# Optimization experiments

Hardware: AMD Instinct MI355X
Metric: run time of the kernel (lower is better)

The kernel has to match this reference:

```python
import jax, jax.numpy as jnp
import numpy as np

N, C, H, W = 4, 128, 64, 64


def setup_inputs() -> dict:
    key = jax.random.key(0)
    ks = jax.random.split(key, 4)
    s = 1.0 / np.sqrt(C).astype(np.float32)  # conv2d default-init scale
    return {
        "x": jax.random.normal(ks[0], (N, C, H, W), dtype=jnp.float32),
        "Wq": jax.random.normal(ks[1], (C, C), dtype=jnp.float32) * s,
        "bq": jnp.zeros((C,), dtype=jnp.float32),
        "Wk": jax.random.normal(ks[2], (C, C), dtype=jnp.float32) * s,
        "bk": jnp.zeros((C,), dtype=jnp.float32),
        "Wv": jax.random.normal(ks[3], (C, C), dtype=jnp.float32) * s,
        "bv": jnp.zeros((C,), dtype=jnp.float32),
    }


def reference(x, Wq, bq, Wk, bk, Wv, bv):
    n, c, h, w = x.shape
    xf = x.reshape(n, c, h * w)  # [N, C, L], L = H*W
    # 1x1 convs == per-pixel channel mixing
    q = jnp.einsum('oc,ncl->nol', Wq, xf) + bq[:, None]
    k = jnp.einsum('oc,ncl->nol', Wk, xf) + bk[:, None]
    v = jnp.einsum('oc,ncl->nol', Wv, xf) + bv[:, None]
    # scores[l, m] = sum_c k[c,l] * q[c,m]  (matmul(k^T, q))
    scale = jnp.asarray(1.0 / np.sqrt(c), x.dtype)
    scores = jnp.einsum('ncl,ncm->nlm', k, q) * scale  # [N, L, L]
    temp = jax.nn.softmax(scores, axis=-1)
    attn = jnp.einsum('ncl,nlm->ncm', v, temp)  # [N, C, L]
    return x + attn.reshape(n, c, h, w)
```

## Files before the change

### kernel.cpp

```cpp
#include <hip/hip_runtime.h>
#include <hip/hip_bf16.h>
#include <stdint.h>

#define NB 4
#define CH 128
#define LL 4096

typedef __attribute__((ext_vector_type(8))) short short8;
typedef __attribute__((ext_vector_type(4))) short short4b;
typedef __attribute__((ext_vector_type(4))) float floatx4;
typedef __attribute__((ext_vector_type(16))) float floatx16;


static __device__ __forceinline__ short f2bf(float f) {
    uint32_t u = __float_as_uint(f);
    u += 0x7fffu + ((u >> 16) & 1u);
    return (short)(u >> 16);
}
static __device__ __forceinline__ float bf2f(short s) {
    return __uint_as_float(((uint32_t)(uint16_t)s) << 16);
}

__global__ __launch_bounds__(256) void wprep_kernel(
    const float* __restrict__ Wq, const float* __restrict__ Wk,
    const float* __restrict__ Wv, short* __restrict__ Wf)
{
    const int g = blockIdx.x * 256 + threadIdx.x;
    const int mat = g >> 14;
    const int rem = g & 16383;
    const int o   = rem >> 7;
    const int c   = rem & 127;
    const float* W = (mat == 0) ? Wq : (mat == 1) ? Wk : Wv;
    float v = W[o * CH + c];
    if (mat == 1) v *= 0.08838834764831845f;
    Wf[(size_t)mat * 16384 + (o >> 4) * 2048 + (c >> 5) * 512
       + ((c >> 3) & 3) * 128 + (o & 15) * 8 + (c & 7)] = f2bf(v);
}

__global__ __launch_bounds__(256) void proj_kernel(
    const float* __restrict__ x, const short* __restrict__ Wf,
    const float* __restrict__ bq, const float* __restrict__ bk,
    const float* __restrict__ bv,
    short* __restrict__ Qf, short* __restrict__ Kf, short* __restrict__ Vp)
{
    const int i    = blockIdx.x;
    const int n    = (i >> 1) & 3;
    const int lt   = ((i >> 3) << 1) | (i & 1);
    const int l0   = lt << 5;
    const int tid  = threadIdx.x;
    const int wave = tid >> 6;
    const int lane = tid & 63;
    const int quad = lane >> 4;
    const int mc   = lane & 15;

    __shared__ short Xb[32][136];

    {
        const int sl = tid & 31;
        const int cg = tid >> 5;
        const float* xp = x + ((size_t)n * CH + cg * 16) * LL + l0 + sl;
        short8 buf;
        #pragma unroll
        for (int i2 = 0; i2 < 16; ++i2) {
            buf[i2 & 7] = f2bf(xp[(size_t)i2 * LL]);
            if ((i2 & 7) == 7)
                *(short8*)(void*)&Xb[sl][cg * 16 + (i2 & 8)] = buf;
        }
    }
    __syncthreads();

    const int lt2 = wave >> 1;
    const int oh  = wave & 1;
    const int gt  = lt * 2 + lt2;

    short8 xf[4];
    #pragma unroll
    for (int s = 0; s < 4; ++s)
        xf[s] = *(const short8*)(const void*)&Xb[lt2 * 16 + mc][32 * s + quad * 8];

    const size_t obase = ((size_t)n * 256 + gt) * 2048;
    const float scale = 0.08838834764831845f;

    #pragma unroll
    for (int mat = 0; mat < 3; ++mat) {
        const short* Wm = Wf + (size_t)mat * 16384;
        const float* bb = (mat == 0) ? bq : (mat == 1) ? bk : bv;
        const float bscale = (mat == 1) ? scale : 1.0f;
        #pragma unroll
        for (int ot = oh * 4; ot < oh * 4 + 4; ++ot) {
            floatx4 acc = {0.f, 0.f, 0.f, 0.f};
            #pragma unroll
            for (int s = 0; s < 4; ++s)
                acc = __builtin_amdgcn_mfma_f32_16x16x32_bf16(
                    *(const short8*)(const void*)(Wm + ot * 2048 + s * 512 + lane * 8),
                    xf[s], acc, 0, 0, 0);
            const int c0 = ot * 16 + 4 * quad;
            if (mat < 2) {
                short4b pv;
                #pragma unroll
                for (int r = 0; r < 4; ++r)
                    pv[r] = f2bf(acc[r] + bb[c0 + r] * bscale);
                short* dst = ((mat == 0) ? Qf : Kf) + obase
                           + (c0 >> 5) * 512 + ((c0 >> 3) & 3) * 128
                           + mc * 8 + (c0 & 7);
                *(short4b*)(void*)dst = pv;
            } else {
                #pragma unroll
                for (int r = 0; r < 4; ++r)
                    Vp[obase + (c0 + r) * 16 + mc] = f2bf(acc[r] + bb[c0 + r]);
            }
        }
    }
}

__global__ __launch_bounds__(1024) void rowsum_kernel(
    const short* __restrict__ Qf, const short* __restrict__ Kf,
    float* __restrict__ Dv)
{
    const int i    = blockIdx.x;
    const int n    = (i >> 1) & 3;
    const int tq   = ((i >> 3) << 1) | (i & 1);
    const int tid  = threadIdx.x;
    const int wave = tid >> 6;
    const int lane = tid & 63;
    const int quad = lane >> 4;
    const int mc   = lane & 15;
    const int mw   = wave & 7;
    const int th   = wave >> 3;

    __shared__ float Db[16][32];

    const short* Kb = Kf + ((size_t)n * 256 + tq * 4 + th * 2) * 2048 + lane * 8;
    short8 kf[2][4];
    #pragma unroll
    for (int t = 0; t < 2; ++t)
        #pragma unroll
        for (int s = 0; s < 4; ++s)
            kf[t][s] = *(const short8*)(const void*)(Kb + t * 2048 + s * 512);

    const short* Qn = Qf + (size_t)n * 524288 + (size_t)mw * 32 * 2048 + lane * 8;
    float rs[2][4] = {{0.f, 0.f, 0.f, 0.f}, {0.f, 0.f, 0.f, 0.f}};

    short8 qA[4], qB[4];
    #pragma unroll
    for (int s = 0; s < 4; ++s)
        qA[s] = *(const short8*)(const void*)(Qn + s * 512);

    auto qstep = [&](const short8 (&q)[4]) {
        floatx4 a0 = {0.f, 0.f, 0.f, 0.f};
        floatx4 a1 = {0.f, 0.f, 0.f, 0.f};
        #pragma unroll
        for (int s = 0; s < 4; ++s) {
            a0 = __builtin_amdgcn_mfma_f32_16x16x32_bf16(kf[0][s], q[s], a0, 0, 0, 0);
            a1 = __builtin_amdgcn_mfma_f32_16x16x32_bf16(kf[1][s], q[s], a1, 0, 0, 0);
        }
        #pragma unroll
        for (int r = 0; r < 4; ++r) {
            rs[0][r] += __expf(a0[r]);
            rs[1][r] += __expf(a1[r]);
        }
    };

    for (int it = 0; it < 32; it += 2) {
        #pragma unroll
        for (int s = 0; s < 4; ++s)
            qB[s] = *(const short8*)(const void*)(
                Qn + (size_t)((it + 1) & 31) * 2048 + s * 512);
        qstep(qA);
        #pragma unroll
        for (int s = 0; s < 4; ++s)
            qA[s] = *(const short8*)(const void*)(
                Qn + (size_t)((it + 2) & 31) * 2048 + s * 512);
        qstep(qB);
    }

    #pragma unroll
    for (int t = 0; t < 2; ++t)
        #pragma unroll
        for (int r = 0; r < 4; ++r) {
            float v = rs[t][r];
            v += __shfl_xor(v, 1);
            v += __shfl_xor(v, 2);
            v += __shfl_xor(v, 4);
            v += __shfl_xor(v, 8);
            if (mc == 0) Db[wave][t * 16 + quad * 4 + r] = v;
        }
    __syncthreads();
    if (tid < 64) {
        const int lh = tid >> 5, lr = tid & 31;
        float s = 0.f;
        #pragma unroll
        for (int m = 0; m < 8; ++m) s += Db[lh * 8 + m][lr];
        Dv[(size_t)n * 4096 + tq * 64 + tid] = 1.0f / s;
    }
}

__global__ __launch_bounds__(1024) void attn_out_kernel(
    const short* __restrict__ Qf, const short* __restrict__ Kf,
    const short* __restrict__ Vp, const float* __restrict__ Dv,
    const float* __restrict__ x, float* __restrict__ out)
{
    const int i    = blockIdx.x;
    const int n    = (i >> 1) & 3;
    const int mb   = ((i >> 3) << 1) | (i & 1);
    const int m0   = mb << 6;
    const int tid  = threadIdx.x;
    const int wave = tid >> 6;
    const int lane = tid & 63;
    const int quad = lane >> 4;
    const int mc   = lane & 15;
    const int l32  = lane & 31;
    const int h    = lane >> 5;
    const int ct   = wave & 3;
    const int mh   = (wave >> 2) & 1;
    const int kh   = wave >> 3;

    __shared__ short P[2][64][264];
    __shared__ float Rbuf[4][2][64][16];

    const short* Qn  = Qf + (size_t)n * 524288;
    const short* Kn  = Kf + (size_t)n * 524288;
    const short* Vpn = Vp + (size_t)n * 524288;
    const float* Dn  = Dv + (size_t)n * 4096;

    short8 qf[4][4];
    #pragma unroll
    for (int mst = 0; mst < 4; ++mst)
        #pragma unroll
        for (int s = 0; s < 4; ++s)
            qf[mst][s] = *(const short8*)(const void*)(
                Qn + (size_t)((m0 >> 4) + mst) * 2048 + s * 512 + lane * 8);

    floatx16 acc;
    #pragma unroll
    for (int r = 0; r < 16; ++r) acc[r] = 0.f;

    for (int step = 0; step < 16; ++step) {
        const int lb = step << 8;
        const int p  = step & 1;

        short8 kfr[4];
        #pragma unroll
        for (int s = 0; s < 4; ++s)
            kfr[s] = *(const short8*)(const void*)(
                Kn + (size_t)(step * 16 + wave) * 2048 + s * 512 + lane * 8);
        const floatx4 dr = *(const floatx4*)(const void*)(
            Dn + lb + wave * 16 + quad * 4);

        #pragma unroll
        for (int mst = 0; mst < 4; ++mst) {
            floatx4 sa = {0.f, 0.f, 0.f, 0.f};
            #pragma unroll
            for (int s = 0; s < 4; ++s)
                sa = __builtin_amdgcn_mfma_f32_16x16x32_bf16(kfr[s], qf[mst][s], sa, 0, 0, 0);
            short4b pv;
            #pragma unroll
            for (int r = 0; r < 4; ++r) pv[r] = f2bf(__expf(sa[r]) * dr[r]);
            *(short4b*)(void*)&P[p][16 * mst + mc][16 * wave + quad * 4] = pv;
        }
        __syncthreads();

        #pragma unroll
        for (int i2 = 0; i2 < 8; ++i2) {
            const int kc = kh * 8 + i2;
            const short8 vf = *(const short8*)(const void*)(
                Vpn + (size_t)((lb >> 4) + kc) * 2048 + (32 * ct + l32) * 16 + 8 * h);
            const short8 pf = *(const short8*)(const void*)&P[p][32 * mh + l32][16 * kc + 8 * h];
            acc = __builtin_amdgcn_mfma_f32_32x32x16_bf16(vf, pf, acc, 0, 0, 0);
        }
    }

    __syncthreads();
    if (kh == 1)
        *(floatx16*)(void*)&Rbuf[ct][mh][lane][0] = acc;
    __syncthreads();
    if (kh == 0) {
        const floatx16 o = *(const floatx16*)(const void*)&Rbuf[ct][mh][lane][0];
        #pragma unroll
        for (int r = 0; r < 16; ++r) {
            const int c = 32 * ct + (r & 3) + 8 * (r >> 2) + 4 * h;
            const int m = m0 + 32 * mh + l32;
            const size_t idx = ((size_t)n * CH + c) * LL + m;
            out[idx] = x[idx] + acc[r] + o[r];
        }
    }
}

extern "C" void kernel_launch(void* const* d_in, const int* in_sizes, int n_in,
                              void* d_out, int out_size, void* d_ws, size_t ws_size,
                              hipStream_t stream) {
    (void)in_sizes; (void)n_in; (void)out_size; (void)ws_size;
    const float* x  = (const float*)d_in[0];
    const float* Wq = (const float*)d_in[1];
    const float* bq = (const float*)d_in[2];
    const float* Wk = (const float*)d_in[3];
    const float* bk = (const float*)d_in[4];
    const float* Wv = (const float*)d_in[5];
    const float* bv = (const float*)d_in[6];
    float* out = (float*)d_out;

    char* ws = (char*)d_ws;
    short* Qf = (short*)(ws);
    short* Kf = (short*)(ws + 4194304);
    short* Vp = (short*)(ws + 8388608);
    float* Dv = (float*)(ws + 12582912);
    short* Wf = (short*)(ws + 16777216);

    wprep_kernel<<<192, 256, 0, stream>>>(Wq, Wk, Wv, Wf);
    proj_kernel<<<512, 256, 0, stream>>>(x, Wf, bq, bk, bv, Qf, Kf, Vp);
    rowsum_kernel<<<256, 1024, 0, stream>>>(Qf, Kf, Dv);
    attn_out_kernel<<<256, 1024, 0, stream>>>(Qf, Kf, Vp, Dv, x, out);
}
```

Measured before the change: 169.2 us.

## Halve attn_out tile to 32 queries, 512 threads, prefetch next K/D and V

The attention-output kernel now processes 32 query columns per block with 8 waves (512 threads) instead of 64 columns with 16 waves, doubling the grid to 512 blocks. Each step covers 128 keys, and the K fragments and row-sum reciprocals for the next step are loaded during the current step's compute. V fragments are loaded into registers before the score MFMAs, so their latency overlaps with the exp/P work. The reduction buffer now reuses the P shared array. The intent is more blocks per CU and better hiding of global-load latency, at the cost of more register pressure and more total K/V reads, since each block now covers fewer queries.

```diff
diff --git a/kernel.cpp b/kernel.cpp
--- a/kernel.cpp
+++ b/kernel.cpp
@@ -195,7 +195,7 @@
     }
 }
 
-__global__ __launch_bounds__(1024) void attn_out_kernel(
+__global__ __launch_bounds__(512, 4) void attn_out_kernel(
     const short* __restrict__ Qf, const short* __restrict__ Kf,
     const short* __restrict__ Vp, const float* __restrict__ Dv,
     const float* __restrict__ x, float* __restrict__ out)
@@ -203,7 +203,7 @@
     const int i    = blockIdx.x;
     const int n    = (i >> 1) & 3;
     const int mb   = ((i >> 3) << 1) | (i & 1);
-    const int m0   = mb << 6;
+    const int m0   = mb << 5;
     const int tid  = threadIdx.x;
     const int wave = tid >> 6;
     const int lane = tid & 63;
@@ -212,20 +212,19 @@
     const int l32  = lane & 31;
     const int h    = lane >> 5;
     const int ct   = wave & 3;
-    const int mh   = (wave >> 2) & 1;
-    const int kh   = wave >> 3;
-
-    __shared__ short P[2][64][264];
-    __shared__ float Rbuf[4][2][64][16];
+    const int kh   = wave >> 2;
+
+    __shared__ short P[2][32][138];
+    float* Rb = (float*)&P[0][0][0];
 
     const short* Qn  = Qf + (size_t)n * 524288;
     const short* Kn  = Kf + (size_t)n * 524288;
     const short* Vpn = Vp + (size_t)n * 524288;
     const float* Dn  = Dv + (size_t)n * 4096;
 
-    short8 qf[4][4];
-    #pragma unroll
-    for (int mst = 0; mst < 4; ++mst)
+    short8 qf[2][4];
+    #pragma unroll
+    for (int mst = 0; mst < 2; ++mst)
         #pragma unroll
         for (int s = 0; s < 4; ++s)
             qf[mst][s] = *(const short8*)(const void*)(
@@ -235,20 +234,35 @@
     #pragma unroll
     for (int r = 0; r < 16; ++r) acc[r] = 0.f;
 
-    for (int step = 0; step < 16; ++step) {
-        const int lb = step << 8;
+    short8 kfr[4];
+    #pragma unroll
+    for (int s = 0; s < 4; ++s)
+        kfr[s] = *(const short8*)(const void*)(
+            Kn + (size_t)wave * 2048 + s * 512 + lane * 8);
+    floatx4 dr = *(const floatx4*)(const void*)(Dn + wave * 16 + quad * 4);
+
+    for (int step = 0; step < 32; ++step) {
+        const int lb = step << 7;
         const int p  = step & 1;
 
-        short8 kfr[4];
-        #pragma unroll
-        for (int s = 0; s < 4; ++s)
-            kfr[s] = *(const short8*)(const void*)(
-                Kn + (size_t)(step * 16 + wave) * 2048 + s * 512 + lane * 8);
-        const floatx4 dr = *(const floatx4*)(const void*)(
-            Dn + lb + wave * 16 + quad * 4);
-
-        #pragma unroll
-        for (int mst = 0; mst < 4; ++mst) {
+        short8 vf[4];
+        #pragma unroll
+        for (int s = 0; s < 4; ++s)
+            vf[s] = *(const short8*)(const void*)(
+                Vpn + (size_t)((lb >> 4) + kh * 4 + s) * 2048
+                    + (32 * ct + l32) * 16 + 8 * h);
+
+        const int sn = (step + 1) & 31;
+        short8 kfn[4];
+        #pragma unroll
+        for (int s = 0; s < 4; ++s)
+            kfn[s] = *(const short8*)(const void*)(
+                Kn + (size_t)(sn * 8 + wave) * 2048 + s * 512 + lane * 8);
+        const floatx4 dn2 = *(const floatx4*)(const void*)(
+            Dn + (sn << 7) + wave * 16 + quad * 4);
+
+        #pragma unroll
+        for (int mst = 0; mst < 2; ++mst) {
             floatx4 sa = {0.f, 0.f, 0.f, 0.f};
             #pragma unroll
             for (int s = 0; s < 4; ++s)
@@ -261,25 +275,27 @@
         __syncthreads();
 
         #pragma unroll
-        for (int i2 = 0; i2 < 8; ++i2) {
-            const int kc = kh * 8 + i2;
-            const short8 vf = *(const short8*)(const void*)(
-                Vpn + (size_t)((lb >> 4) + kc) * 2048 + (32 * ct + l32) * 16 + 8 * h);
-            const short8 pf = *(const short8*)(const void*)&P[p][32 * mh + l32][16 * kc + 8 * h];
-            acc = __builtin_amdgcn_mfma_f32_32x32x16_bf16(vf, pf, acc, 0, 0, 0);
-        }
+        for (int i2 = 0; i2 < 4; ++i2) {
+            const int kc = kh * 4 + i2;
+            const short8 pf = *(const short8*)(const void*)&P[p][l32][16 * kc + 8 * h];
+            acc = __builtin_amdgcn_mfma_f32_32x32x16_bf16(vf[i2], pf, acc, 0, 0, 0);
+        }
+
+        #pragma unroll
+        for (int s = 0; s < 4; ++s) kfr[s] = kfn[s];
+        dr = dn2;
     }
 
     __syncthreads();
     if (kh == 1)
-        *(floatx16*)(void*)&Rbuf[ct][mh][lane][0] = acc;
+        *(floatx16*)(void*)&Rb[(ct * 64 + lane) * 16] = acc;
     __syncthreads();
     if (kh == 0) {
-        const floatx16 o = *(const floatx16*)(const void*)&Rbuf[ct][mh][lane][0];
+        const floatx16 o = *(const floatx16*)(const void*)&Rb[(ct * 64 + lane) * 16];
         #pragma unroll
         for (int r = 0; r < 16; ++r) {
             const int c = 32 * ct + (r & 3) + 8 * (r >> 2) + 4 * h;
-            const int m = m0 + 32 * mh + l32;
+            const int m = m0 + l32;
             const size_t idx = ((size_t)n * CH + c) * LL + m;
             out[idx] = x[idx] + acc[r] + o[r];
         }
@@ -309,5 +325,5 @@
     wprep_kernel<<<192, 256, 0, stream>>>(Wq, Wk, Wv, Wf);
     proj_kernel<<<512, 256, 0, stream>>>(x, Wf, bq, bk, bv, Qf, Kf, Vp);
     rowsum_kernel<<<256, 1024, 0, stream>>>(Qf, Kf, Dv);
-    attn_out_kernel<<<256, 1024, 0, stream>>>(Qf, Kf, Vp, Dv, x, out);
-}
+    attn_out_kernel<<<512, 512, 0, stream>>>(Qf, Kf, Vp, Dv, x, out);
+}
```

Result: slower. 191.6 us (+13.2%).

## Software-pipeline attention loop: compute next P tile while consuming current

Applied to the files above, without the earlier changes.

Restructures the main loop so that the score/exp tile for step t+1 is computed into the alternate P buffer while the PV MFMAs for step t run, with a prologue that computes the first tile. K and D loads are prefetched two steps ahead and V fragments are loaded into registers ahead of use, and the loop now needs one barrier per iteration instead of sitting on one between the two phases. This aims to hide global-load latency and overlap the two MFMA phases, at the cost of higher register pressure from the extra prefetched fragments, which could reduce occupancy.

```diff
diff --git a/kernel.cpp b/kernel.cpp
--- a/kernel.cpp
+++ b/kernel.cpp
@@ -235,42 +235,93 @@
     #pragma unroll
     for (int r = 0; r < 16; ++r) acc[r] = 0.f;
 
-    for (int step = 0; step < 16; ++step) {
-        const int lb = step << 8;
-        const int p  = step & 1;
-
-        short8 kfr[4];
-        #pragma unroll
-        for (int s = 0; s < 4; ++s)
-            kfr[s] = *(const short8*)(const void*)(
-                Kn + (size_t)(step * 16 + wave) * 2048 + s * 512 + lane * 8);
-        const floatx4 dr = *(const floatx4*)(const void*)(
-            Dn + lb + wave * 16 + quad * 4);
-
-        #pragma unroll
-        for (int mst = 0; mst < 4; ++mst) {
-            floatx4 sa = {0.f, 0.f, 0.f, 0.f};
+    short8 knxt[4];
+    #pragma unroll
+    for (int s = 0; s < 4; ++s)
+        knxt[s] = *(const short8*)(const void*)(
+            Kn + (size_t)wave * 2048 + s * 512 + lane * 8);
+    floatx4 dnxt = *(const floatx4*)(const void*)(Dn + wave * 16 + quad * 4);
+
+    #pragma unroll
+    for (int mst = 0; mst < 4; ++mst) {
+        floatx4 sa = {0.f, 0.f, 0.f, 0.f};
+        #pragma unroll
+        for (int s = 0; s < 4; ++s)
+            sa = __builtin_amdgcn_mfma_f32_16x16x32_bf16(knxt[s], qf[mst][s], sa, 0, 0, 0);
+        short4b pv;
+        #pragma unroll
+        for (int r = 0; r < 4; ++r) pv[r] = f2bf(__expf(sa[r]) * dnxt[r]);
+        *(short4b*)(void*)&P[0][16 * mst + mc][16 * wave + quad * 4] = pv;
+    }
+    #pragma unroll
+    for (int s = 0; s < 4; ++s)
+        knxt[s] = *(const short8*)(const void*)(
+            Kn + (size_t)(16 + wave) * 2048 + s * 512 + lane * 8);
+    dnxt = *(const floatx4*)(const void*)(Dn + 256 + wave * 16 + quad * 4);
+    __syncthreads();
+
+    #pragma unroll 2
+    for (int t = 0; t < 16; ++t) {
+        const int lb = t << 8;
+        const int p  = t & 1;
+
+        short8 vf0[4];
+        #pragma unroll
+        for (int s = 0; s < 4; ++s)
+            vf0[s] = *(const short8*)(const void*)(
+                Vpn + (size_t)((lb >> 4) + kh * 8 + s) * 2048
+                    + (32 * ct + l32) * 16 + 8 * h);
+
+        const int tf = (t + 2 < 16) ? t + 2 : 15;
+        short8 kfut[4];
+        #pragma unroll
+        for (int s = 0; s < 4; ++s)
+            kfut[s] = *(const short8*)(const void*)(
+                Kn + (size_t)(tf * 16 + wave) * 2048 + s * 512 + lane * 8);
+        const floatx4 dfut = *(const floatx4*)(const void*)(
+            Dn + (tf << 8) + wave * 16 + quad * 4);
+
+        if (t < 15) {
             #pragma unroll
-            for (int s = 0; s < 4; ++s)
-                sa = __builtin_amdgcn_mfma_f32_16x16x32_bf16(kfr[s], qf[mst][s], sa, 0, 0, 0);
-            short4b pv;
-            #pragma unroll
-            for (int r = 0; r < 4; ++r) pv[r] = f2bf(__expf(sa[r]) * dr[r]);
-            *(short4b*)(void*)&P[p][16 * mst + mc][16 * wave + quad * 4] = pv;
-        }
+            for (int mst = 0; mst < 4; ++mst) {
+                floatx4 sa = {0.f, 0.f, 0.f, 0.f};
+                #pragma unroll
+                for (int s = 0; s < 4; ++s)
+                    sa = __builtin_amdgcn_mfma_f32_16x16x32_bf16(knxt[s], qf[mst][s], sa, 0, 0, 0);
+                short4b pv;
+                #pragma unroll
+                for (int r = 0; r < 4; ++r) pv[r] = f2bf(__expf(sa[r]) * dnxt[r]);
+                *(short4b*)(void*)&P[p ^ 1][16 * mst + mc][16 * wave + quad * 4] = pv;
+            }
+        }
+
+        short8 vf1[4];
+        #pragma unroll
+        for (int s = 0; s < 4; ++s)
+            vf1[s] = *(const short8*)(const void*)(
+                Vpn + (size_t)((lb >> 4) + kh * 8 + 4 + s) * 2048
+                    + (32 * ct + l32) * 16 + 8 * h);
+
+        #pragma unroll
+        for (int i2 = 0; i2 < 4; ++i2) {
+            const int kc = kh * 8 + i2;
+            const short8 pf = *(const short8*)(const void*)&P[p][32 * mh + l32][16 * kc + 8 * h];
+            acc = __builtin_amdgcn_mfma_f32_32x32x16_bf16(vf0[i2], pf, acc, 0, 0, 0);
+        }
+        #pragma unroll
+        for (int i2 = 0; i2 < 4; ++i2) {
+            const int kc = kh * 8 + 4 + i2;
+            const short8 pf = *(const short8*)(const void*)&P[p][32 * mh + l32][16 * kc + 8 * h];
+            acc = __builtin_amdgcn_mfma_f32_32x32x16_bf16(vf1[i2], pf, acc, 0, 0, 0);
+        }
+
         __syncthreads();
 
         #pragma unroll
-        for (int i2 = 0; i2 < 8; ++i2) {
-            const int kc = kh * 8 + i2;
-            const short8 vf = *(const short8*)(const void*)(
-                Vpn + (size_t)((lb >> 4) + kc) * 2048 + (32 * ct + l32) * 16 + 8 * h);
-            const short8 pf = *(const short8*)(const void*)&P[p][32 * mh + l32][16 * kc + 8 * h];
-            acc = __builtin_amdgcn_mfma_f32_32x32x16_bf16(vf, pf, acc, 0, 0, 0);
-        }
-    }
-
-    __syncthreads();
+        for (int s = 0; s < 4; ++s) knxt[s] = kfut[s];
+        dnxt = dfut;
+    }
+
     if (kh == 1)
         *(floatx16*)(void*)&Rbuf[ct][mh][lane][0] = acc;
     __syncthreads();
```

New measurement: 203.3 us. 1.2x slower.

## Split attention reduction across blocks and add combine kernel for partial outputs

Applied to the files above, without the earlier changes.

The attention-output kernel drops the in-block split of the key dimension across wave halves. It instead splits the key range across two separate blocks, each writing a partial fp32 output to workspace, and a new combine kernel adds x and both partials. The rowsum and attention kernels move from 1024-thread to 512-thread blocks, with twice as many blocks and a launch-bounds occupancy hint of 4. The aim is more blocks and higher occupancy per CU. The cost is an extra kernel launch, extra global traffic for the partial outputs, and Q fragments reloaded inside the loop instead of being held in registers.

```diff
diff --git a/kernel.cpp b/kernel.cpp
--- a/kernel.cpp
+++ b/kernel.cpp
@@ -113,24 +113,22 @@
     }
 }
 
-__global__ __launch_bounds__(1024) void rowsum_kernel(
+__global__ __launch_bounds__(512, 4) void rowsum_kernel(
     const short* __restrict__ Qf, const short* __restrict__ Kf,
     float* __restrict__ Dv)
 {
     const int i    = blockIdx.x;
     const int n    = (i >> 1) & 3;
-    const int tq   = ((i >> 3) << 1) | (i & 1);
+    const int tp   = ((i >> 3) << 1) | (i & 1);
     const int tid  = threadIdx.x;
     const int wave = tid >> 6;
     const int lane = tid & 63;
     const int quad = lane >> 4;
     const int mc   = lane & 15;
-    const int mw   = wave & 7;
-    const int th   = wave >> 3;
-
-    __shared__ float Db[16][32];
-
-    const short* Kb = Kf + ((size_t)n * 256 + tq * 4 + th * 2) * 2048 + lane * 8;
+
+    __shared__ float Db[8][32];
+
+    const short* Kb = Kf + ((size_t)n * 256 + tp * 2) * 2048 + lane * 8;
     short8 kf[2][4];
     #pragma unroll
     for (int t = 0; t < 2; ++t)
@@ -138,7 +136,7 @@
         for (int s = 0; s < 4; ++s)
             kf[t][s] = *(const short8*)(const void*)(Kb + t * 2048 + s * 512);
 
-    const short* Qn = Qf + (size_t)n * 524288 + (size_t)mw * 32 * 2048 + lane * 8;
+    const short* Qn = Qf + (size_t)n * 524288 + (size_t)wave * 32 * 2048 + lane * 8;
     float rs[2][4] = {{0.f, 0.f, 0.f, 0.f}, {0.f, 0.f, 0.f, 0.f}};
 
     short8 qA[4], qB[4];
@@ -186,23 +184,24 @@
             if (mc == 0) Db[wave][t * 16 + quad * 4 + r] = v;
         }
     __syncthreads();
-    if (tid < 64) {
-        const int lh = tid >> 5, lr = tid & 31;
+    if (tid < 32) {
         float s = 0.f;
         #pragma unroll
-        for (int m = 0; m < 8; ++m) s += Db[lh * 8 + m][lr];
-        Dv[(size_t)n * 4096 + tq * 64 + tid] = 1.0f / s;
-    }
-}
-
-__global__ __launch_bounds__(1024) void attn_out_kernel(
+        for (int m = 0; m < 8; ++m) s += Db[m][tid];
+        Dv[(size_t)n * 4096 + tp * 32 + tid] = 1.0f / s;
+    }
+}
+
+__global__ __launch_bounds__(512, 4) void attn_out_kernel(
     const short* __restrict__ Qf, const short* __restrict__ Kf,
     const short* __restrict__ Vp, const float* __restrict__ Dv,
-    const float* __restrict__ x, float* __restrict__ out)
+    float* __restrict__ Po)
 {
     const int i    = blockIdx.x;
     const int n    = (i >> 1) & 3;
-    const int mb   = ((i >> 3) << 1) | (i & 1);
+    const int j    = ((i >> 3) << 1) | (i & 1);
+    const int lh   = j >> 6;
+    const int mb   = j & 63;
     const int m0   = mb << 6;
     const int tid  = threadIdx.x;
     const int wave = tid >> 6;
@@ -212,78 +211,95 @@
     const int l32  = lane & 31;
     const int h    = lane >> 5;
     const int ct   = wave & 3;
-    const int mh   = (wave >> 2) & 1;
-    const int kh   = wave >> 3;
+    const int mh   = wave >> 2;
 
     __shared__ short P[2][64][264];
-    __shared__ float Rbuf[4][2][64][16];
 
     const short* Qn  = Qf + (size_t)n * 524288;
     const short* Kn  = Kf + (size_t)n * 524288;
     const short* Vpn = Vp + (size_t)n * 524288;
     const float* Dn  = Dv + (size_t)n * 4096;
-
-    short8 qf[4][4];
-    #pragma unroll
-    for (int mst = 0; mst < 4; ++mst)
-        #pragma unroll
-        for (int s = 0; s < 4; ++s)
-            qf[mst][s] = *(const short8*)(const void*)(
-                Qn + (size_t)((m0 >> 4) + mst) * 2048 + s * 512 + lane * 8);
+    const int tile0  = lh * 128;
 
     floatx16 acc;
     #pragma unroll
     for (int r = 0; r < 16; ++r) acc[r] = 0.f;
 
-    for (int step = 0; step < 16; ++step) {
-        const int lb = step << 8;
-        const int p  = step & 1;
-
-        short8 kfr[4];
-        #pragma unroll
-        for (int s = 0; s < 4; ++s)
-            kfr[s] = *(const short8*)(const void*)(
-                Kn + (size_t)(step * 16 + wave) * 2048 + s * 512 + lane * 8);
-        const floatx4 dr = *(const floatx4*)(const void*)(
-            Dn + lb + wave * 16 + quad * 4);
-
-        #pragma unroll
-        for (int mst = 0; mst < 4; ++mst) {
-            floatx4 sa = {0.f, 0.f, 0.f, 0.f};
+    for (int t = 0; t < 8; ++t) {
+        const int p = t & 1;
+
+        {
+            const int tb = tile0 + t * 16 + 2 * wave;
+            short8 kfr[2][4];
             #pragma unroll
-            for (int s = 0; s < 4; ++s)
-                sa = __builtin_amdgcn_mfma_f32_16x16x32_bf16(kfr[s], qf[mst][s], sa, 0, 0, 0);
-            short4b pv;
+            for (int jj = 0; jj < 2; ++jj)
+                #pragma unroll
+                for (int s = 0; s < 4; ++s)
+                    kfr[jj][s] = *(const short8*)(const void*)(
+                        Kn + (size_t)(tb + jj) * 2048 + s * 512 + lane * 8);
+            floatx4 dr[2];
             #pragma unroll
-            for (int r = 0; r < 4; ++r) pv[r] = f2bf(__expf(sa[r]) * dr[r]);
-            *(short4b*)(void*)&P[p][16 * mst + mc][16 * wave + quad * 4] = pv;
+            for (int jj = 0; jj < 2; ++jj)
+                dr[jj] = *(const floatx4*)(const void*)(
+                    Dn + (tb + jj) * 16 + quad * 4);
+
+            #pragma unroll
+            for (int mst = 0; mst < 4; ++mst) {
+                short8 qt[4];
+                #pragma unroll
+                for (int s = 0; s < 4; ++s)
+                    qt[s] = *(const short8*)(const void*)(
+                        Qn + (size_t)((m0 >> 4) + mst) * 2048 + s * 512 + lane * 8);
+                floatx4 sa0 = {0.f, 0.f, 0.f, 0.f};
+                floatx4 sa1 = {0.f, 0.f, 0.f, 0.f};
+                #pragma unroll
+                for (int s = 0; s < 4; ++s) {
+                    sa0 = __builtin_amdgcn_mfma_f32_16x16x32_bf16(kfr[0][s], qt[s], sa0, 0, 0, 0);
+                    sa1 = __builtin_amdgcn_mfma_f32_16x16x32_bf16(kfr[1][s], qt[s], sa1, 0, 0, 0);
+                }
+                short4b pv0, pv1;
+                #pragma unroll
+                for (int r = 0; r < 4; ++r) {
+                    pv0[r] = f2bf(__expf(sa0[r]) * dr[0][r]);
+                    pv1[r] = f2bf(__expf(sa1[r]) * dr[1][r]);
+                }
+                *(short4b*)(void*)&P[p][16 * mst + mc][32 * wave + quad * 4] = pv0;
+                *(short4b*)(void*)&P[p][16 * mst + mc][32 * wave + 16 + quad * 4] = pv1;
+            }
         }
         __syncthreads();
 
         #pragma unroll
-        for (int i2 = 0; i2 < 8; ++i2) {
-            const int kc = kh * 8 + i2;
+        for (int kc = 0; kc < 16; ++kc) {
             const short8 vf = *(const short8*)(const void*)(
-                Vpn + (size_t)((lb >> 4) + kc) * 2048 + (32 * ct + l32) * 16 + 8 * h);
+                Vpn + (size_t)(tile0 + t * 16 + kc) * 2048
+                    + (32 * ct + l32) * 16 + 8 * h);
             const short8 pf = *(const short8*)(const void*)&P[p][32 * mh + l32][16 * kc + 8 * h];
             acc = __builtin_amdgcn_mfma_f32_32x32x16_bf16(vf, pf, acc, 0, 0, 0);
         }
     }
 
-    __syncthreads();
-    if (kh == 1)
-        *(floatx16*)(void*)&Rbuf[ct][mh][lane][0] = acc;
-    __syncthreads();
-    if (kh == 0) {
-        const floatx16 o = *(const floatx16*)(const void*)&Rbuf[ct][mh][lane][0];
-        #pragma unroll
-        for (int r = 0; r < 16; ++r) {
-            const int c = 32 * ct + (r & 3) + 8 * (r >> 2) + 4 * h;
-            const int m = m0 + 32 * mh + l32;
-            const size_t idx = ((size_t)n * CH + c) * LL + m;
-            out[idx] = x[idx] + acc[r] + o[r];
-        }
-    }
+    float* Pon = Po + (size_t)(lh * 4 + n) * 524288;
+    #pragma unroll
+    for (int r = 0; r < 16; ++r) {
+        const int c = 32 * ct + (r & 3) + 8 * (r >> 2) + 4 * h;
+        const int m = m0 + 32 * mh + l32;
+        Pon[(size_t)c * LL + m] = acc[r];
+    }
+}
+
+__global__ __launch_bounds__(256) void combine_kernel(
+    const float* __restrict__ x, const float* __restrict__ Po,
+    float* __restrict__ out)
+{
+    const size_t k = (size_t)blockIdx.x * 256 + threadIdx.x;
+    const floatx4 a = *(const floatx4*)(const void*)(x + 4 * k);
+    const floatx4 b = *(const floatx4*)(const void*)(Po + 4 * k);
+    const floatx4 c = *(const floatx4*)(const void*)(Po + 2097152 + 4 * k);
+    floatx4 o;
+    #pragma unroll
+    for (int r = 0; r < 4; ++r) o[r] = a[r] + b[r] + c[r];
+    *(floatx4*)(void*)(out + 4 * k) = o;
 }
 
 extern "C" void kernel_launch(void* const* d_in, const int* in_sizes, int n_in,
@@ -305,9 +321,11 @@
     short* Vp = (short*)(ws + 8388608);
     float* Dv = (float*)(ws + 12582912);
     short* Wf = (short*)(ws + 16777216);
+    float* Po = (float*)(ws + 16908288);
 
     wprep_kernel<<<192, 256, 0, stream>>>(Wq, Wk, Wv, Wf);
     proj_kernel<<<512, 256, 0, stream>>>(x, Wf, bq, bk, bv, Qf, Kf, Vp);
-    rowsum_kernel<<<256, 1024, 0, stream>>>(Qf, Kf, Dv);
-    attn_out_kernel<<<256, 1024, 0, stream>>>(Qf, Kf, Vp, Dv, x, out);
-}
+    rowsum_kernel<<<512, 512, 0, stream>>>(Qf, Kf, Dv);
+    attn_out_kernel<<<512, 512, 0, stream>>>(Qf, Kf, Vp, Dv, Po);
+    combine_kernel<<<2048, 256, 0, stream>>>(x, Po, out);
+}
```

Result: faster. 157.8 us (-6.7%).
